# Optimization experiments

Measured on AMD Instinct MI355X. Metric: run time of the kernel, lower is better.

## Reference

```python
import jax, jax.numpy as jnp
import numpy as np

B, T = 64, 128
IN, H, L, OUT = 512, 1024, 2, 1


def _gru_scan(seq, Wi, Wh, bi, bh):
    # seq: (S, in_dim); PyTorch GRU cell, gate order r, z, n.
    h0 = jnp.zeros((H,), dtype=seq.dtype)
    def step(h, x):
        gi = x @ Wi.T + bi          # (3H,)
        gh = h @ Wh.T + bh          # (3H,)
        r = jax.nn.sigmoid(gi[:H] + gh[:H])
        z = jax.nn.sigmoid(gi[H:2 * H] + gh[H:2 * H])
        n = jnp.tanh(gi[2 * H:] + r * gh[2 * H:])
        h_new = (1.0 - z) * n + z * h
        return h_new, h_new
    _, hs = jax.lax.scan(step, h0, seq)
    return hs                        # (S, H)


def setup_inputs() -> dict:
    key = jax.random.key(0)
    ks = jax.random.split(key, 24)
    mk = lambda k, shape: jax.random.normal(k, shape, dtype=jnp.float32) * 0.05
    d = {}
    d['x'] = jax.random.normal(ks[0], (B, T, IN), dtype=jnp.float32)
    # gru1: layer0 input=IN, layer1 input=H
    d['g1_Wi0'] = mk(ks[1], (3 * H, IN)); d['g1_Wh0'] = mk(ks[2], (3 * H, H))
    d['g1_bi0'] = mk(ks[3], (3 * H,));    d['g1_bh0'] = mk(ks[4], (3 * H,))
    d['g1_Wi1'] = mk(ks[5], (3 * H, H));  d['g1_Wh1'] = mk(ks[6], (3 * H, H))
    d['g1_bi1'] = mk(ks[7], (3 * H,));    d['g1_bh1'] = mk(ks[8], (3 * H,))
    # gru2: both layers input=H
    d['g2_Wi0'] = mk(ks[9], (3 * H, H));  d['g2_Wh0'] = mk(ks[10], (3 * H, H))
    d['g2_bi0'] = mk(ks[11], (3 * H,));   d['g2_bh0'] = mk(ks[12], (3 * H,))
    d['g2_Wi1'] = mk(ks[13], (3 * H, H)); d['g2_Wh1'] = mk(ks[14], (3 * H, H))
    d['g2_bi1'] = mk(ks[15], (3 * H,));   d['g2_bh1'] = mk(ks[16], (3 * H,))
    d['fc1_W'] = mk(ks[17], (64, H));     d['fc1_b'] = mk(ks[18], (64,))
    d['fc2_W'] = mk(ks[19], (OUT, 64));   d['fc2_b'] = mk(ks[20], (OUT,))
    return d


def reference(x, g1_Wi0, g1_Wh0, g1_bi0, g1_bh0, g1_Wi1, g1_Wh1, g1_bi1, g1_bh1,
              g2_Wi0, g2_Wh0, g2_bi0, g2_bh0, g2_Wi1, g2_Wh1, g2_bi1, g2_bh1,
              fc1_W, fc1_b, fc2_W, fc2_b):
    # PyTorch feeds x[:, t, :] (2-D) to a batch_first GRU -> treated as an
    # UNBATCHED sequence of length B; hidden is carried across t. That equals
    # one GRU scan over the flattened (T*B)-step sequence, t-major / b-minor.
    seq = jnp.swapaxes(x, 0, 1).reshape(T * B, IN)
    hs0 = _gru_scan(seq, g1_Wi0, g1_Wh0, g1_bi0, g1_bh0)    # (T*B, H) layer 0
    hs1 = _gru_scan(hs0, g1_Wi1, g1_Wh1, g1_bi1, g1_bh1)    # (T*B, H) layer 1
    # h returned after timestep t is the hidden at flat step t*B + (B-1)
    s = jnp.stack([hs0, hs1], axis=1)[B - 1::B]             # (T, L, H)
    seq2 = s.reshape(T * L, H)                              # torch.cat(s)
    # gru2 over the [1, T*L, H] sequence (batch=1)
    hs2_0 = _gru_scan(seq2, g2_Wi0, g2_Wh0, g2_bi0, g2_bh0)
    hs2_1 = _gru_scan(hs2_0, g2_Wi1, g2_Wh1, g2_bi1, g2_bh1)
    h2 = jnp.stack([hs2_0[-1], hs2_1[-1]], axis=0)[:, None, :]  # (L, 1, H)
    y = jax.nn.sigmoid(h2 @ fc1_W.T + fc1_b)                # (L, 1, 64)
    out = jax.nn.sigmoid(y @ fc2_W.T + fc2_b)               # (L, 1, OUT)
    return out
```

## Files before the change

### kernel.cpp

```cpp
#include <hip/hip_runtime.h>


typedef unsigned u32x4 __attribute__((ext_vector_type(4)));
typedef _Float16 h2_t  __attribute__((ext_vector_type(2)));

#define S1 8192
#define S2 256

__device__ u32x4 g_h0s[S1][256];
__device__ u32x4 g_h1s[S1][256];
__device__ u32x4 g_q0s[S2][256];
__device__ u32x4 g_q1s[S2][256];
__device__ unsigned long long g_fast[4][2][512];
__device__ int   g_claim[128];

__device__ __forceinline__ unsigned pk(float a, float b) {
  unsigned short ua = __builtin_bit_cast(unsigned short, (_Float16)a);
  unsigned short ub = __builtin_bit_cast(unsigned short, (_Float16)b);
  return (unsigned)ua | ((unsigned)ub << 16);
}
__device__ __forceinline__ float unpk(unsigned u, int hi) {
  unsigned short us = (unsigned short)(hi ? (u >> 16) : (u & 0xffffu));
  return (float)__builtin_bit_cast(_Float16, us);
}

#if __has_builtin(__builtin_amdgcn_fdot2)
__device__ __forceinline__ float fdot2(unsigned a, unsigned b, float c) {
  return __builtin_amdgcn_fdot2(__builtin_bit_cast(h2_t, a),
                                __builtin_bit_cast(h2_t, b), c, false);
}
#else
__device__ __forceinline__ float fdot2(unsigned a, unsigned b, float c) {
  h2_t ha = __builtin_bit_cast(h2_t, a), hb = __builtin_bit_cast(h2_t, b);
  return c + (float)ha[0] * (float)hb[0] + (float)ha[1] * (float)hb[1];
}
#endif

__device__ __forceinline__ u32x4 ld_sc_v4(const u32x4* p) {
  u32x4 v;
  asm volatile("global_load_dwordx4 %0, %1, off sc1\n\t"
               "s_waitcnt vmcnt(0)" : "=&v"(v) : "v"(p) : "memory");
  return v;
}
__device__ __forceinline__ void ld_sc_4x4(const u32x4* p0, const u32x4* p1,
                                          const u32x4* p2, const u32x4* p3,
                                          u32x4& a, u32x4& b, u32x4& c, u32x4& d) {
  asm volatile("global_load_dwordx4 %0, %4, off sc1\n\t"
               "global_load_dwordx4 %1, %5, off sc1\n\t"
               "global_load_dwordx4 %2, %6, off sc1\n\t"
               "global_load_dwordx4 %3, %7, off sc1\n\t"
               "s_waitcnt vmcnt(0)"
               : "=&v"(a), "=&v"(b), "=&v"(c), "=&v"(d)
               : "v"(p0), "v"(p1), "v"(p2), "v"(p3) : "memory");
}
__device__ __forceinline__ void st_sc_v4(u32x4* p, u32x4 v) {
  asm volatile("global_store_dwordx4 %0, %1, off sc1" :: "v"(p), "v"(v) : "memory");
}

__device__ __forceinline__ float rcpf(float x) {
#if __has_builtin(__builtin_amdgcn_rcpf)
  return __builtin_amdgcn_rcpf(x);
#else
  return 1.f / x;
#endif
}
__device__ __forceinline__ float sigf(float x) { return rcpf(1.f + __expf(-x)); }
__device__ __forceinline__ float tanh_f(float x) {
  x = fminf(fmaxf(x, -15.f), 15.f);
  const float e = __expf(2.f * x);
  return (e - 1.f) * rcpf(e + 1.f);
}

__device__ __forceinline__ int swzHc(int ch) { return ch ^ ((ch >> 3) & 7); }
__device__ __forceinline__ int swzH_pos(int i) { return (swzHc(i >> 2) << 2) | (i & 3); }
__device__ __forceinline__ int swzX_pos(int i) {
  int ch = i >> 2; ch ^= (ch >> 2) & 7; return (ch << 2) | (i & 3);
}

__global__ void init_all() {
  const long long NH = (long long)S1 * 256;
  const long long NQ = (long long)S2 * 256;
  const long long N  = 2 * NH + 2 * NQ;
  u32x4 ff = {0u, 0u, 0xFFFFFFFFu, 0u};
  const long long idx = (long long)blockIdx.x * blockDim.x + threadIdx.x;
  const long long str = (long long)gridDim.x * blockDim.x;
  for (long long k = idx; k < N; k += str) {
    u32x4* r;
    long long k2 = k;
    if (k2 < NH) r = &g_h0s[0][0] + k2;
    else {
      k2 -= NH;
      if (k2 < NH) r = &g_h1s[0][0] + k2;
      else {
        k2 -= NH;
        if (k2 < NQ) r = &g_q0s[0][0] + k2;
        else         r = &g_q1s[0][0] + (k2 - NQ);
      }
    }
    *r = ff;
  }
  for (long long k = idx; k < 4LL * 2 * 512; k += str)
    ((unsigned long long*)g_fast)[k] = 0xFFFFFFFF00000000ULL;
  if (blockIdx.x == 0 && threadIdx.x < 128) g_claim[threadIdx.x] = 0;
}

__device__ __forceinline__ const u32x4* in_addr(int role, int u, int r) {
  if (role == 1) return &g_h0s[u][r];
  if (role == 2) {
    const int ss = ((u >> 1) << 6) + 63;
    return (u & 1) ? &g_h1s[ss][r] : &g_h0s[ss][r];
  }
  return &g_q0s[u][r];
}
__device__ __forceinline__ unsigned in_want(int role, int u) {
  return (role == 2) ? (unsigned)(((u >> 1) << 6) + 63) : (unsigned)u;
}

#define MAC4(A, W4, H4)                                                       \
  A = fdot2((W4)[0], (H4)[0], A); A = fdot2((W4)[1], (H4)[1], A);             \
  A = fdot2((W4)[2], (H4)[2], A); A = fdot2((W4)[3], (H4)[3], A);

#define RED16(A)                                                              \
  A += __shfl_xor(A, 8, 16); A += __shfl_xor(A, 4, 16);                       \
  A += __shfl_xor(A, 2, 16); A += __shfl_xor(A, 1, 16);

#define STREAM_FETCH_WAVE(U, LN)                                              \
  {                                                                           \
    const unsigned w = in_want(role, (U));                                    \
    const u32x4* p0 = in_addr(role, (U), 4 * (LN) + 0);                       \
    const u32x4* p1 = in_addr(role, (U), 4 * (LN) + 1);                       \
    const u32x4* p2 = in_addr(role, (U), 4 * (LN) + 2);                       \
    const u32x4* p3 = in_addr(role, (U), 4 * (LN) + 3);                       \
    u32x4 r0, r1, r2, r3;                                                     \
    ld_sc_4x4(p0, p1, p2, p3, r0, r1, r2, r3);                                \
    while (r0[2] != w || r1[2] != w || r2[2] != w || r3[2] != w)              \
      ld_sc_4x4(p0, p1, p2, p3, r0, r1, r2, r3);                              \
    unsigned* dst = sIN[(U) & 7];                                             \
    const int b8 = 8 * (LN);                                                  \
    dst[swzH_pos(b8 + 0)] = r0[0]; dst[swzH_pos(b8 + 1)] = r0[1];             \
    dst[swzH_pos(b8 + 2)] = r1[0]; dst[swzH_pos(b8 + 3)] = r1[1];             \
    dst[swzH_pos(b8 + 4)] = r2[0]; dst[swzH_pos(b8 + 5)] = r2[1];             \
    dst[swzH_pos(b8 + 6)] = r3[0]; dst[swzH_pos(b8 + 7)] = r3[1];             \
  }

#define X_FETCH_WAVE(U, LN)                                                   \
  {                                                                           \
    const float4* xp = (const float4*)(x +                                    \
        (size_t)(((U) & 63) * 128 + ((U) >> 6)) * 512 + 8 * (LN));            \
    float4 a = xp[0], b = xp[1];                                              \
    unsigned* dst = sX[(U) & 7];                                              \
    const int b4 = 4 * (LN);                                                  \
    dst[swzX_pos(b4 + 0)] = pk(a.x, a.y);                                     \
    dst[swzX_pos(b4 + 1)] = pk(a.z, a.w);                                     \
    dst[swzX_pos(b4 + 2)] = pk(b.x, b.y);                                     \
    dst[swzX_pos(b4 + 3)] = pk(b.z, b.w);                                     \
  }

__global__
__attribute__((amdgpu_flat_work_group_size(512, 512), amdgpu_num_vgpr(256)))
void gru_all(const float* __restrict__ x,
             const float* __restrict__ g1_Wi0, const float* __restrict__ g1_Wh0,
             const float* __restrict__ g1_bi0, const float* __restrict__ g1_bh0,
             const float* __restrict__ g1_Wi1, const float* __restrict__ g1_Wh1,
             const float* __restrict__ g1_bi1, const float* __restrict__ g1_bh1,
             const float* __restrict__ g2_Wi0, const float* __restrict__ g2_Wh0,
             const float* __restrict__ g2_bi0, const float* __restrict__ g2_bh0,
             const float* __restrict__ g2_Wi1, const float* __restrict__ g2_Wh1,
             const float* __restrict__ g2_bi1, const float* __restrict__ g2_bh1,
             const float* __restrict__ fc1W, const float* __restrict__ fc1b,
             const float* __restrict__ fc2W, const float* __restrict__ fc2b,
             float* __restrict__ out)
{
  const int tid = threadIdx.x;
  const int G   = tid >> 4;
  const int q   = tid & 15;
  const int sw  = (tid >> 6) - 4;
  const int ln  = tid & 63;
  const int rid = tid - 256;

  __shared__ __attribute__((aligned(16))) unsigned sH[2][512];
  __shared__ __attribute__((aligned(16))) unsigned sIN[8][512];
  __shared__ __attribute__((aligned(16))) unsigned sX[8][256];
  __shared__ float sD[96];
  __shared__ float sDI[96];
  __shared__ float sY[128];
  __shared__ int   sSlot;

  unsigned xcc;
  asm volatile("s_getreg_b32 %0, hwreg(HW_REG_XCC_ID)" : "=s"(xcc));
  xcc &= 7u;
  if (tid == 0) {
    int slot = -1;
    if (xcc < 4u) {
      for (int i = 0; i < 32 && slot < 0; ++i)
        if (atomicCAS(&g_claim[(int)xcc * 32 + i], 0, 1) == 0)
          slot = (int)xcc * 32 + i;
    }
    if (slot < 0) {
      for (int k = 0; k < 32; ++k) __builtin_amdgcn_s_sleep(64);
      for (int i = 0; i < 128 && slot < 0; ++i)
        if (atomicCAS(&g_claim[i], 0, 1) == 0) slot = i;
    }
    sSlot = slot;
  }
  __syncthreads();
  const int slot = sSlot;
  if (slot < 0) return;
  const int role = slot >> 5;
  const int rank = slot & 31;
  const int e0   = rank * 32;
  const int S    = (role <= 1) ? S1 : S2;

  const float* Wh  = (role == 0) ? g1_Wh0 : (role == 1) ? g1_Wh1
                   : (role == 2) ? g2_Wh0 : g2_Wh1;
  const float* Wi  = (role == 0) ? g1_Wi0 : (role == 1) ? g1_Wi1
                   : (role == 2) ? g2_Wi0 : g2_Wi1;
  const float* pbi = (role == 0) ? g1_bi0 : (role == 1) ? g1_bi1
                   : (role == 2) ? g2_bi0 : g2_bi1;
  const float* pbh = (role == 0) ? g1_bh0 : (role == 1) ? g1_bh1
                   : (role == 2) ? g2_bh0 : g2_bh1;
  u32x4 (*outA)[256] = (role == 0) ? g_h0s : (role == 1) ? g_h1s
                     : (role == 2) ? g_q0s : g_q1s;

  u32x4 wv[6][8];
  {
    const bool isWh = (G < 16);
    const int  Gm   = isWh ? G : (G - 16);
    const float* M  = isWh ? Wh : Wi;
    const bool wide = isWh || (role != 0);
    #pragma unroll
    for (int j = 0; j < 6; ++j) {
      const int rr = Gm * 6 + j;
      const int R  = (rr >> 5) * 1024 + e0 + (rr & 31);
      if (wide) {
        const float4* rp = (const float4*)(M + (size_t)R * 1024 + 64 * q);
        #pragma unroll
        for (int c = 0; c < 8; ++c) {
          float4 a = rp[2 * c], b = rp[2 * c + 1];
          wv[j][c] = (u32x4){pk(a.x, a.y), pk(a.z, a.w), pk(b.x, b.y), pk(b.z, b.w)};
        }
      } else {
        const float4* rp = (const float4*)(M + (size_t)R * 512 + 32 * q);
        #pragma unroll
        for (int c = 0; c < 4; ++c) {
          float4 a = rp[2 * c], b = rp[2 * c + 1];
          wv[j][c] = (u32x4){pk(a.x, a.y), pk(a.z, a.w), pk(b.x, b.y), pk(b.z, b.w)};
        }
      }
    }
  }

  float bIr = 0, bIz = 0, bIn = 0, bHr = 0, bHz = 0, bHn = 0;
  if (tid < 32) {
    const int ge = e0 + tid;
    bIr = pbi[ge]; bIz = pbi[1024 + ge]; bIn = pbi[2048 + ge];
    bHr = pbh[ge]; bHz = pbh[1024 + ge]; bHn = pbh[2048 + ge];
  }

  if (tid >= 256) {
    const int u = sw;
    if (role == 0) { X_FETCH_WAVE(u, ln); }
    else           { STREAM_FETCH_WAVE(u, ln); }
  }
  __syncthreads();

  for (int s = 0; s < S; ++s) {
    const int par = s & 1;

    if (tid >= 256 && (s & 3) == 0) {
      const int u = s + 4 + sw;
      if (u < S) {
        if (role == 0) { X_FETCH_WAVE(u, ln); }
        else           { STREAM_FETCH_WAVE(u, ln); }
      }
    }

    if (tid < 256) {
      unsigned d0 = 0, d1 = 0;
      if (s > 0) {
        const unsigned w = (unsigned)(s - 1);
        unsigned long long* f0 = &g_fast[role][(s - 1) & 1][2 * tid];
        unsigned long long* f1 = f0 + 1;
        unsigned long long v0 = atomicAdd(f0, 0ull);
        unsigned long long v1 = atomicAdd(f1, 0ull);
        bool o0 = ((unsigned)(v0 >> 32) == w), o1 = ((unsigned)(v1 >> 32) == w);
        while (!(o0 && o1)) {
          if (!o0) v0 = atomicAdd(f0, 0ull);
          if (!o1) v1 = atomicAdd(f1, 0ull);
          o0 = ((unsigned)(v0 >> 32) == w); o1 = ((unsigned)(v1 >> 32) == w);
        }
        d0 = (unsigned)v0; d1 = (unsigned)v1;
      }
      sH[par][swzH_pos(2 * tid)]     = d0;
      sH[par][swzH_pos(2 * tid + 1)] = d1;
    }
    __syncthreads();

    float a0 = 0, a1 = 0, a2 = 0, a3 = 0, a4 = 0, a5 = 0;
    if (G < 16) {
      const u32x4* HV = (const u32x4*)sH[par];
      #pragma unroll
      for (int c = 0; c < 8; ++c) {
        const u32x4 h4 = HV[8 * q + (c ^ (q & 7))];
        MAC4(a0, wv[0][c], h4); MAC4(a1, wv[1][c], h4); MAC4(a2, wv[2][c], h4);
        MAC4(a3, wv[3][c], h4); MAC4(a4, wv[4][c], h4); MAC4(a5, wv[5][c], h4);
      }
    } else if (role != 0) {
      const u32x4* IV = (const u32x4*)sIN[s & 7];
      #pragma unroll
      for (int c = 0; c < 8; ++c) {
        const u32x4 h4 = IV[8 * q + (c ^ (q & 7))];
        MAC4(a0, wv[0][c], h4); MAC4(a1, wv[1][c], h4); MAC4(a2, wv[2][c], h4);
        MAC4(a3, wv[3][c], h4); MAC4(a4, wv[4][c], h4); MAC4(a5, wv[5][c], h4);
      }
    } else {
      const u32x4* XV = (const u32x4*)sX[s & 7];
      #pragma unroll
      for (int c = 0; c < 4; ++c) {
        const int ch = 4 * q + c;
        const u32x4 h4 = XV[ch ^ ((ch >> 2) & 7)];
        MAC4(a0, wv[0][c], h4); MAC4(a1, wv[1][c], h4); MAC4(a2, wv[2][c], h4);
        MAC4(a3, wv[3][c], h4); MAC4(a4, wv[4][c], h4); MAC4(a5, wv[5][c], h4);
      }
    }
    RED16(a0); RED16(a1); RED16(a2); RED16(a3); RED16(a4); RED16(a5);
    if (q < 6) {
      const float v = (q == 0) ? a0 : (q == 1) ? a1 : (q == 2) ? a2
                    : (q == 3) ? a3 : (q == 4) ? a4 : a5;
      if (G < 16) sD[G * 6 + q] = v;
      else        sDI[(G - 16) * 6 + q] = v;
    }
    __syncthreads();

    if (tid < 32) {
      const float rg = sigf(sDI[tid] + bIr + sD[tid] + bHr);
      const float zg = sigf(sDI[32 + tid] + bIz + sD[32 + tid] + bHz);
      const float ng = tanh_f(sDI[64 + tid] + bIn + rg * (sD[64 + tid] + bHn));
      const int ge = e0 + tid;
      const float hp = unpk(sH[par][swzH_pos(ge >> 1)], ge & 1);
      const float hn = (1.f - zg) * ng + zg * hp;
      const int i2 = (tid & 15) * 2;
      const float p0 = __shfl(hn, i2), p1 = __shfl(hn, i2 + 1);
      const int b4 = (tid & 7) * 4;
      const float v0 = __shfl(hn, b4),     v1 = __shfl(hn, b4 + 1);
      const float v2 = __shfl(hn, b4 + 2), v3 = __shfl(hn, b4 + 3);
      if (tid < 16) {
        unsigned long long val =
            ((unsigned long long)(unsigned)s << 32) | (unsigned long long)pk(p0, p1);
        atomicExch(&g_fast[role][s & 1][rank * 16 + tid], val);
      }
      if (tid < 8) {
        u32x4 rec = {pk(v0, v1), pk(v2, v3), (unsigned)s, 0u};
        st_sc_v4(&outA[s][rank * 8 + tid], rec);
      }
    }
  }

  if (role == 3 && rank == 0) {
    if (tid < 256) {
      const u32x4* a = &g_q0s[S2 - 1][tid];
      u32x4 r = ld_sc_v4(a);
      while (r[2] != (unsigned)(S2 - 1)) r = ld_sc_v4(a);
      sH[0][swzH_pos(2 * tid)]     = r[0];
      sH[0][swzH_pos(2 * tid + 1)] = r[1];
    } else {
      const u32x4* a = &g_q1s[S2 - 1][rid];
      u32x4 r = ld_sc_v4(a);
      while (r[2] != (unsigned)(S2 - 1)) r = ld_sc_v4(a);
      sH[1][swzH_pos(2 * rid)]     = r[0];
      sH[1][swzH_pos(2 * rid + 1)] = r[1];
    }
    __syncthreads();
    if (tid < 128) {
      const int l = tid >> 6, k = tid & 63;
      const unsigned* Hs = (const unsigned*)sH[l];
      const float* wrow = fc1W + (size_t)k * 1024;
      float acc = fc1b[k];
      for (int j2 = 0; j2 < 512; ++j2) {
        const unsigned hu = Hs[swzH_pos(j2)];
        acc += unpk(hu, 0) * wrow[2 * j2] + unpk(hu, 1) * wrow[2 * j2 + 1];
      }
      sY[tid] = sigf(acc);
    }
    __syncthreads();
    if (tid < 2) {
      const float* yv = sY + tid * 64;
      float acc = fc2b[0];
      for (int k2 = 0; k2 < 64; ++k2) acc += fc2W[k2] * yv[k2];
      out[tid] = sigf(acc);
    }
  }
}

extern "C" void kernel_launch(void* const* d_in, const int* in_sizes, int n_in,
                              void* d_out, int out_size, void* d_ws, size_t ws_size,
                              hipStream_t stream) {
  (void)in_sizes; (void)n_in; (void)out_size; (void)d_ws; (void)ws_size;
  const float* x      = (const float*)d_in[0];
  const float* g1_Wi0 = (const float*)d_in[1];
  const float* g1_Wh0 = (const float*)d_in[2];
  const float* g1_bi0 = (const float*)d_in[3];
  const float* g1_bh0 = (const float*)d_in[4];
  const float* g1_Wi1 = (const float*)d_in[5];
  const float* g1_Wh1 = (const float*)d_in[6];
  const float* g1_bi1 = (const float*)d_in[7];
  const float* g1_bh1 = (const float*)d_in[8];
  const float* g2_Wi0 = (const float*)d_in[9];
  const float* g2_Wh0 = (const float*)d_in[10];
  const float* g2_bi0 = (const float*)d_in[11];
  const float* g2_bh0 = (const float*)d_in[12];
  const float* g2_Wi1 = (const float*)d_in[13];
  const float* g2_Wh1 = (const float*)d_in[14];
  const float* g2_bi1 = (const float*)d_in[15];
  const float* g2_bh1 = (const float*)d_in[16];
  const float* fc1W   = (const float*)d_in[17];
  const float* fc1b   = (const float*)d_in[18];
  const float* fc2W   = (const float*)d_in[19];
  const float* fc2b   = (const float*)d_in[20];
  float* out = (float*)d_out;

  init_all<<<dim3(2048), dim3(256), 0, stream>>>();
  gru_all<<<dim3(256), dim3(512), 0, stream>>>(
      x, g1_Wi0, g1_Wh0, g1_bi0, g1_bh0, g1_Wi1, g1_Wh1, g1_bi1, g1_bh1,
      g2_Wi0, g2_Wh0, g2_bi0, g2_bh0, g2_Wi1, g2_Wh1, g2_bi1, g2_bh1,
      fc1W, fc1b, fc2W, fc2b, out);
}
```

Before: 25.36 ms.

## Replace per-element tagged flag polling with a global step counter barrier

Each block used to spin on 512 tagged 64-bit atomics per step to collect the previous hidden state. Now a single thread polls one per-role counter until all 32 blocks have published the step, then every block reads the hidden vector directly from the outA records. Producers fence and bump the counter after storing. The change also adds s_sleep backoff to the spin loops and swaps the fixed VGPR cap for a waves_per_eu hint. The goal is less atomic traffic, at the cost of an extra serialized counter wait and an extra block barrier on each step.

```diff
diff --git a/kernel.cpp b/kernel.cpp
--- a/kernel.cpp
+++ b/kernel.cpp
@@ -11,7 +11,7 @@
 __device__ u32x4 g_h1s[S1][256];
 __device__ u32x4 g_q0s[S2][256];
 __device__ u32x4 g_q1s[S2][256];
-__device__ unsigned long long g_fast[4][2][512];
+__device__ unsigned g_cnt[4];
 __device__ int   g_claim[128];
 
 __device__ __forceinline__ unsigned pk(float a, float b) {
@@ -41,6 +41,13 @@
   asm volatile("global_load_dwordx4 %0, %1, off sc1\n\t"
                "s_waitcnt vmcnt(0)" : "=&v"(v) : "v"(p) : "memory");
   return v;
+}
+__device__ __forceinline__ void ld_sc_2x4(const u32x4* p0, const u32x4* p1,
+                                          u32x4& a, u32x4& b) {
+  asm volatile("global_load_dwordx4 %0, %2, off sc1\n\t"
+               "global_load_dwordx4 %1, %3, off sc1\n\t"
+               "s_waitcnt vmcnt(0)"
+               : "=&v"(a), "=&v"(b) : "v"(p0), "v"(p1) : "memory");
 }
 __device__ __forceinline__ void ld_sc_4x4(const u32x4* p0, const u32x4* p1,
                                           const u32x4* p2, const u32x4* p3,
@@ -99,9 +106,10 @@
     }
     *r = ff;
   }
-  for (long long k = idx; k < 4LL * 2 * 512; k += str)
-    ((unsigned long long*)g_fast)[k] = 0xFFFFFFFF00000000ULL;
-  if (blockIdx.x == 0 && threadIdx.x < 128) g_claim[threadIdx.x] = 0;
+  if (blockIdx.x == 0) {
+    if (threadIdx.x < 128) g_claim[threadIdx.x] = 0;
+    if (threadIdx.x < 4)   g_cnt[threadIdx.x] = 0u;
+  }
 }
 
 __device__ __forceinline__ const u32x4* in_addr(int role, int u, int r) {
@@ -133,8 +141,10 @@
     const u32x4* p3 = in_addr(role, (U), 4 * (LN) + 3);                       \
     u32x4 r0, r1, r2, r3;                                                     \
     ld_sc_4x4(p0, p1, p2, p3, r0, r1, r2, r3);                                \
-    while (r0[2] != w || r1[2] != w || r2[2] != w || r3[2] != w)              \
+    while (r0[2] != w || r1[2] != w || r2[2] != w || r3[2] != w) {            \
+      __builtin_amdgcn_s_sleep(8);                                            \
       ld_sc_4x4(p0, p1, p2, p3, r0, r1, r2, r3);                              \
+    }                                                                         \
     unsigned* dst = sIN[(U) & 7];                                             \
     const int b8 = 8 * (LN);                                                  \
     dst[swzH_pos(b8 + 0)] = r0[0]; dst[swzH_pos(b8 + 1)] = r0[1];             \
@@ -157,7 +167,7 @@
   }
 
 __global__
-__attribute__((amdgpu_flat_work_group_size(512, 512), amdgpu_num_vgpr(256)))
+__attribute__((amdgpu_flat_work_group_size(512, 512), amdgpu_waves_per_eu(2, 2)))
 void gru_all(const float* __restrict__ x,
              const float* __restrict__ g1_Wi0, const float* __restrict__ g1_Wh0,
              const float* __restrict__ g1_bi0, const float* __restrict__ g1_bh0,
@@ -275,24 +285,39 @@
       }
     }
 
+    if (tid == 0 && s > 0) {
+      const unsigned want = 32u * (unsigned)s;
+      unsigned c = atomicAdd(&g_cnt[role], 0u);
+      while (c < want) {
+        __builtin_amdgcn_s_sleep(2);
+        c = atomicAdd(&g_cnt[role], 0u);
+      }
+    }
+    __syncthreads();
+
     if (tid < 256) {
-      unsigned d0 = 0, d1 = 0;
+      unsigned d0 = 0, d1 = 0, d2 = 0, d3 = 0;
       if (s > 0) {
-        const unsigned w = (unsigned)(s - 1);
-        unsigned long long* f0 = &g_fast[role][(s - 1) & 1][2 * tid];
-        unsigned long long* f1 = f0 + 1;
-        unsigned long long v0 = atomicAdd(f0, 0ull);
-        unsigned long long v1 = atomicAdd(f1, 0ull);
-        bool o0 = ((unsigned)(v0 >> 32) == w), o1 = ((unsigned)(v1 >> 32) == w);
-        while (!(o0 && o1)) {
-          if (!o0) v0 = atomicAdd(f0, 0ull);
-          if (!o1) v1 = atomicAdd(f1, 0ull);
-          o0 = ((unsigned)(v0 >> 32) == w); o1 = ((unsigned)(v1 >> 32) == w);
+        const u32x4* a0 = &outA[s - 1][2 * (tid & 127)];
+        const u32x4* a1 = a0 + 1;
+        u32x4 r0, r1;
+        ld_sc_2x4(a0, a1, r0, r1);
+        if (tid < 128) { d0 = r0[0]; d1 = r0[1]; d2 = r1[0]; d3 = r1[1]; }
+        else           { d0 = r0[0]; d1 = r0[1]; d2 = r1[0]; d3 = r1[1]; }
+        const int base = 4 * (tid & 127);
+        if (tid < 128) {
+          sH[par][swzH_pos(base + 0)] = d0;
+          sH[par][swzH_pos(base + 1)] = d1;
+          sH[par][swzH_pos(base + 2)] = d2;
+          sH[par][swzH_pos(base + 3)] = d3;
         }
-        d0 = (unsigned)v0; d1 = (unsigned)v1;
-      }
-      sH[par][swzH_pos(2 * tid)]     = d0;
-      sH[par][swzH_pos(2 * tid + 1)] = d1;
+      } else if (tid < 128) {
+        const int base = 4 * tid;
+        sH[par][swzH_pos(base + 0)] = 0u;
+        sH[par][swzH_pos(base + 1)] = 0u;
+        sH[par][swzH_pos(base + 2)] = 0u;
+        sH[par][swzH_pos(base + 3)] = 0u;
+      }
     }
     __syncthreads();
 
@@ -339,20 +364,16 @@
       const int ge = e0 + tid;
       const float hp = unpk(sH[par][swzH_pos(ge >> 1)], ge & 1);
       const float hn = (1.f - zg) * ng + zg * hp;
-      const int i2 = (tid & 15) * 2;
-      const float p0 = __shfl(hn, i2), p1 = __shfl(hn, i2 + 1);
       const int b4 = (tid & 7) * 4;
       const float v0 = __shfl(hn, b4),     v1 = __shfl(hn, b4 + 1);
       const float v2 = __shfl(hn, b4 + 2), v3 = __shfl(hn, b4 + 3);
-      if (tid < 16) {
-        unsigned long long val =
-            ((unsigned long long)(unsigned)s << 32) | (unsigned long long)pk(p0, p1);
-        atomicExch(&g_fast[role][s & 1][rank * 16 + tid], val);
-      }
       if (tid < 8) {
         u32x4 rec = {pk(v0, v1), pk(v2, v3), (unsigned)s, 0u};
         st_sc_v4(&outA[s][rank * 8 + tid], rec);
       }
+      asm volatile("s_waitcnt vmcnt(0)" ::: "memory");
+      __threadfence();
+      if (tid == 0) atomicAdd(&g_cnt[role], 1u);
     }
   }
 
@@ -360,13 +381,13 @@
     if (tid < 256) {
       const u32x4* a = &g_q0s[S2 - 1][tid];
       u32x4 r = ld_sc_v4(a);
-      while (r[2] != (unsigned)(S2 - 1)) r = ld_sc_v4(a);
+      while (r[2] != (unsigned)(S2 - 1)) { __builtin_amdgcn_s_sleep(8); r = ld_sc_v4(a); }
       sH[0][swzH_pos(2 * tid)]     = r[0];
       sH[0][swzH_pos(2 * tid + 1)] = r[1];
     } else {
       const u32x4* a = &g_q1s[S2 - 1][rid];
       u32x4 r = ld_sc_v4(a);
-      while (r[2] != (unsigned)(S2 - 1)) r = ld_sc_v4(a);
+      while (r[2] != (unsigned)(S2 - 1)) { __builtin_amdgcn_s_sleep(8); r = ld_sc_v4(a); }
       sH[1][swzH_pos(2 * rid)]     = r[0];
       sH[1][swzH_pos(2 * rid + 1)] = r[1];
     }
```

Result: slower. 62.23 ms (+145.4%).

## Replace per-step atomic hidden exchange with pipelined sc1 polling of flag-tagged records

Applied to the files above, without the earlier changes.

Drops the separate g_fast 64-bit atomic mailbox that broadcast the hidden state between blocks each step. One wave now polls the flag-tagged 16-byte records already written to outA, keeping four sc1 loads in flight and checking them in turn until every record carries the expected step tag. It also adds s_sleep backoff to the other spin loops and swaps the VGPR cap for waves_per_eu(2,2). The aim is to cut atomic round-trip latency and redundant stores on the serial critical path, at the risk of extra polling traffic and of relying on 16-byte loads seeing each tagged record whole.

```diff
diff --git a/kernel.cpp b/kernel.cpp
--- a/kernel.cpp
+++ b/kernel.cpp
@@ -11,7 +11,6 @@
 __device__ u32x4 g_h1s[S1][256];
 __device__ u32x4 g_q0s[S2][256];
 __device__ u32x4 g_q1s[S2][256];
-__device__ unsigned long long g_fast[4][2][512];
 __device__ int   g_claim[128];
 
 __device__ __forceinline__ unsigned pk(float a, float b) {
@@ -99,8 +98,6 @@
     }
     *r = ff;
   }
-  for (long long k = idx; k < 4LL * 2 * 512; k += str)
-    ((unsigned long long*)g_fast)[k] = 0xFFFFFFFF00000000ULL;
   if (blockIdx.x == 0 && threadIdx.x < 128) g_claim[threadIdx.x] = 0;
 }
 
@@ -133,8 +130,10 @@
     const u32x4* p3 = in_addr(role, (U), 4 * (LN) + 3);                       \
     u32x4 r0, r1, r2, r3;                                                     \
     ld_sc_4x4(p0, p1, p2, p3, r0, r1, r2, r3);                                \
-    while (r0[2] != w || r1[2] != w || r2[2] != w || r3[2] != w)              \
+    while (r0[2] != w || r1[2] != w || r2[2] != w || r3[2] != w) {            \
+      __builtin_amdgcn_s_sleep(8);                                            \
       ld_sc_4x4(p0, p1, p2, p3, r0, r1, r2, r3);                              \
+    }                                                                         \
     unsigned* dst = sIN[(U) & 7];                                             \
     const int b8 = 8 * (LN);                                                  \
     dst[swzH_pos(b8 + 0)] = r0[0]; dst[swzH_pos(b8 + 1)] = r0[1];             \
@@ -157,7 +156,7 @@
   }
 
 __global__
-__attribute__((amdgpu_flat_work_group_size(512, 512), amdgpu_num_vgpr(256)))
+__attribute__((amdgpu_flat_work_group_size(512, 512), amdgpu_waves_per_eu(2, 2)))
 void gru_all(const float* __restrict__ x,
              const float* __restrict__ g1_Wi0, const float* __restrict__ g1_Wh0,
              const float* __restrict__ g1_bi0, const float* __restrict__ g1_bh0,
@@ -275,24 +274,56 @@
       }
     }
 
-    if (tid < 256) {
-      unsigned d0 = 0, d1 = 0;
+    if (tid < 64) {
       if (s > 0) {
         const unsigned w = (unsigned)(s - 1);
-        unsigned long long* f0 = &g_fast[role][(s - 1) & 1][2 * tid];
-        unsigned long long* f1 = f0 + 1;
-        unsigned long long v0 = atomicAdd(f0, 0ull);
-        unsigned long long v1 = atomicAdd(f1, 0ull);
-        bool o0 = ((unsigned)(v0 >> 32) == w), o1 = ((unsigned)(v1 >> 32) == w);
-        while (!(o0 && o1)) {
-          if (!o0) v0 = atomicAdd(f0, 0ull);
-          if (!o1) v1 = atomicAdd(f1, 0ull);
-          o0 = ((unsigned)(v0 >> 32) == w); o1 = ((unsigned)(v1 >> 32) == w);
+        const u32x4* p0 = &outA[s - 1][4 * tid + 0];
+        const u32x4* p1 = &outA[s - 1][4 * tid + 1];
+        const u32x4* p2 = &outA[s - 1][4 * tid + 2];
+        const u32x4* p3 = &outA[s - 1][4 * tid + 3];
+        u32x4 r0, r1, r2, r3;
+        asm volatile("global_load_dwordx4 %0, %4, off sc1\n\t"
+                     "global_load_dwordx4 %1, %5, off sc1\n\t"
+                     "global_load_dwordx4 %2, %6, off sc1\n\t"
+                     "global_load_dwordx4 %3, %7, off sc1"
+                     : "=&v"(r0), "=&v"(r1), "=&v"(r2), "=&v"(r3)
+                     : "v"(p0), "v"(p1), "v"(p2), "v"(p3) : "memory");
+        bool done = false;
+        while (!done) {
+          asm volatile("s_waitcnt vmcnt(3)" ::: "memory");
+          __builtin_amdgcn_sched_barrier(0);
+          const bool k0 = (r0[2] == w);
+          asm volatile("global_load_dwordx4 %0, %1, off sc1"
+                       : "=&v"(r0) : "v"(p0) : "memory");
+          asm volatile("s_waitcnt vmcnt(3)" ::: "memory");
+          __builtin_amdgcn_sched_barrier(0);
+          const bool k1 = (r1[2] == w);
+          asm volatile("global_load_dwordx4 %0, %1, off sc1"
+                       : "=&v"(r1) : "v"(p1) : "memory");
+          asm volatile("s_waitcnt vmcnt(3)" ::: "memory");
+          __builtin_amdgcn_sched_barrier(0);
+          const bool k2 = (r2[2] == w);
+          asm volatile("global_load_dwordx4 %0, %1, off sc1"
+                       : "=&v"(r2) : "v"(p2) : "memory");
+          asm volatile("s_waitcnt vmcnt(3)" ::: "memory");
+          __builtin_amdgcn_sched_barrier(0);
+          const bool k3 = (r3[2] == w);
+          asm volatile("global_load_dwordx4 %0, %1, off sc1"
+                       : "=&v"(r3) : "v"(p3) : "memory");
+          done = __all(k0 && k1 && k2 && k3);
         }
-        d0 = (unsigned)v0; d1 = (unsigned)v1;
-      }
-      sH[par][swzH_pos(2 * tid)]     = d0;
-      sH[par][swzH_pos(2 * tid + 1)] = d1;
+        asm volatile("s_waitcnt vmcnt(0)" ::: "memory");
+        __builtin_amdgcn_sched_barrier(0);
+        const int b8 = 8 * tid;
+        sH[par][swzH_pos(b8 + 0)] = r0[0]; sH[par][swzH_pos(b8 + 1)] = r0[1];
+        sH[par][swzH_pos(b8 + 2)] = r1[0]; sH[par][swzH_pos(b8 + 3)] = r1[1];
+        sH[par][swzH_pos(b8 + 4)] = r2[0]; sH[par][swzH_pos(b8 + 5)] = r2[1];
+        sH[par][swzH_pos(b8 + 6)] = r3[0]; sH[par][swzH_pos(b8 + 7)] = r3[1];
+      } else {
+        const int b8 = 8 * tid;
+        #pragma unroll
+        for (int j = 0; j < 8; ++j) sH[par][swzH_pos(b8 + j)] = 0u;
+      }
     }
     __syncthreads();
 
@@ -339,16 +370,9 @@
       const int ge = e0 + tid;
       const float hp = unpk(sH[par][swzH_pos(ge >> 1)], ge & 1);
       const float hn = (1.f - zg) * ng + zg * hp;
-      const int i2 = (tid & 15) * 2;
-      const float p0 = __shfl(hn, i2), p1 = __shfl(hn, i2 + 1);
       const int b4 = (tid & 7) * 4;
       const float v0 = __shfl(hn, b4),     v1 = __shfl(hn, b4 + 1);
       const float v2 = __shfl(hn, b4 + 2), v3 = __shfl(hn, b4 + 3);
-      if (tid < 16) {
-        unsigned long long val =
-            ((unsigned long long)(unsigned)s << 32) | (unsigned long long)pk(p0, p1);
-        atomicExch(&g_fast[role][s & 1][rank * 16 + tid], val);
-      }
       if (tid < 8) {
         u32x4 rec = {pk(v0, v1), pk(v2, v3), (unsigned)s, 0u};
         st_sc_v4(&outA[s][rank * 8 + tid], rec);
@@ -360,13 +384,13 @@
     if (tid < 256) {
       const u32x4* a = &g_q0s[S2 - 1][tid];
       u32x4 r = ld_sc_v4(a);
-      while (r[2] != (unsigned)(S2 - 1)) r = ld_sc_v4(a);
+      while (r[2] != (unsigned)(S2 - 1)) { __builtin_amdgcn_s_sleep(8); r = ld_sc_v4(a); }
       sH[0][swzH_pos(2 * tid)]     = r[0];
       sH[0][swzH_pos(2 * tid + 1)] = r[1];
     } else {
       const u32x4* a = &g_q1s[S2 - 1][rid];
       u32x4 r = ld_sc_v4(a);
-      while (r[2] != (unsigned)(S2 - 1)) r = ld_sc_v4(a);
+      while (r[2] != (unsigned)(S2 - 1)) { __builtin_amdgcn_s_sleep(8); r = ld_sc_v4(a); }
       sH[1][swzH_pos(2 * rid)]     = r[0];
       sH[1][swzH_pos(2 * rid + 1)] = r[1];
     }
```

New measurement: 29.42 ms. 16.0% more time.
